# Kernel tuning notes

Measured on AMD Instinct MI355X. Metric: run time of the kernel, lower is better.

## Reference

```python
import jax, jax.numpy as jnp
import numpy as np

B, N, E, C, M = 4, 16384, 65536, 256, 64

def setup_inputs() -> dict:
    key = jax.random.key(0)
    ks = jax.random.split(key, 12)
    s = 1.0 / np.sqrt(C)
    return {
        'x': jax.random.normal(ks[0], (B, N, C), jnp.float32),
        'edge_attr': jax.random.normal(ks[1], (B, E, 1), jnp.float32),
        'edge_idx': jax.random.randint(ks[2], (B, E, 2), 0, N, jnp.int32),
        'W_fx': jax.random.normal(ks[3], (C, C), jnp.float32) * s,
        'b_fx': jnp.zeros((C,), jnp.float32),
        'W_x': jax.random.normal(ks[4], (C, C), jnp.float32) * s,
        'b_x': jnp.zeros((C,), jnp.float32),
        'W_slice': jax.random.normal(ks[5], (C, M), jnp.float32) * s,
        'b_slice': jnp.zeros((M,), jnp.float32),
        'temp_x': jnp.full((1, 1, M), 0.5, jnp.float32),
        'ph_x': jax.random.uniform(ks[6], (1, 1, C), jnp.float32) / C,
        'W_fedge': jax.random.normal(ks[7], (1, C), jnp.float32),
        'b_fedge': jnp.zeros((C,), jnp.float32),
        'temp_edge': jnp.full((1, 1, M), 0.5, jnp.float32),
        'W_eslice': jax.random.normal(ks[8], (M, M), jnp.float32) * (1.0 / np.sqrt(M)),
        'b_eslice': jnp.zeros((M,), jnp.float32),
        'ph_edge': jax.random.uniform(ks[9], (1, 1, C), jnp.float32) / C,
    }


def reference(x, edge_attr, edge_idx, W_fx, b_fx, W_x, b_x, W_slice, b_slice,
              temp_x, ph_x, W_fedge, b_fedge, temp_edge, W_eslice, b_eslice, ph_edge):
    # node path
    fx_mid = x @ W_fx + b_fx                                  # [B,N,C]
    x_mid = x @ W_x + b_x + ph_x                              # [B,N,C]
    logits = (x_mid @ W_slice + b_slice) / jnp.clip(temp_x, 0.01, 5.0)
    slice_weight = jax.nn.softmax(logits, axis=-1)            # [B,N,M]
    slice_norm = slice_weight.sum(axis=-2)[..., None]         # [B,M,1]
    slice_token = jnp.einsum('bnm,bnc->bmc', slice_weight, fx_mid)
    # edge path
    fedge_mid = edge_attr @ W_fedge + b_fedge + ph_edge       # [B,E,C]
    gather = jax.vmap(lambda sw, idx: sw[idx])                # per-batch node gather
    sw_sum = gather(slice_weight, edge_idx[:, :, 0]) + gather(slice_weight, edge_idx[:, :, 1])
    e_logits = (sw_sum / jnp.clip(temp_edge, 0.01, 5.0)) @ W_eslice + b_eslice
    edge_slice_weight = jax.nn.softmax(e_logits, axis=-1)     # [B,E,M]
    edge_slice_norm = edge_slice_weight.sum(axis=-2)[..., None]
    edge_slice_token = jnp.einsum('bnm,bnc->bmc', edge_slice_weight, fedge_mid)
    scale = x.shape[1] / edge_attr.shape[1]
    slice_token = slice_token + edge_slice_token * scale
    slice_norm = slice_norm + edge_slice_norm * scale
    slice_token = slice_token / (slice_norm + 1e-5)
    return (slice_token, slice_weight)
```

## Files before the change

kernel.cpp:

```cpp
#include <hip/hip_runtime.h>

#define BB 4
#define NN 16384
#define EE 65536
#define CC 256
#define MM 64

#define WS_NORM   0
#define WS_T1     256
#define WS_ESN    512
#define WS_BCOMB  768
#define WS_ITX    832
#define WS_ITE    896
#define WS_WES2   1024
#define WS_WCOMB  5120
#define WS_WES2T  13312
#define WS_SW2    21504
#define WS_SSUM   WS_SW2
#define WS_SPART  4215808

typedef __attribute__((ext_vector_type(8))) __bf16 bf16x8_t;
typedef __attribute__((ext_vector_type(4))) float f32x4_t;

static __device__ __forceinline__ unsigned short f2bf(float f) {
    unsigned int u = __float_as_uint(f);
    unsigned int r = (u + 0x7FFFu + ((u >> 16) & 1u)) >> 16;
    return (unsigned short)r;
}

__global__ __launch_bounds__(256) void kPP(const float* __restrict__ Wx,
                                           const float* __restrict__ Wsl,
                                           const float* __restrict__ bx,
                                           const float* __restrict__ phx,
                                           const float* __restrict__ bsl,
                                           const float* __restrict__ tx,
                                           const float* __restrict__ te,
                                           const float* __restrict__ Wes,
                                           float* __restrict__ ws) {
    __shared__ float row[256];
    __shared__ float part[4][64];
    const int tid = threadIdx.x;
    const int m = tid & 63, kq = tid >> 6;
    if (blockIdx.x < 256) {
        const int c = blockIdx.x;
        row[tid] = Wx[c * CC + tid];
        __syncthreads();
        float acc = 0.f;
#pragma unroll 8
        for (int kk = 0; kk < 64; ++kk) {
            int k = kq * 64 + kk;
            acc += row[k] * Wsl[k * MM + m];
        }
        part[kq][m] = acc;
        __syncthreads();
        if (tid < 64) {
            float v = part[0][tid] + part[1][tid] + part[2][tid] + part[3][tid];
            ((unsigned short*)(ws + WS_WCOMB))[tid * 256 + c] = f2bf(v);
        }
    } else {
#pragma unroll
        for (int i = 0; i < 3; ++i) ws[i * 256 + tid] = 0.f;
        row[tid] = bx[tid] + phx[tid];
        __syncthreads();
        float acc = 0.f;
#pragma unroll 8
        for (int kk = 0; kk < 64; ++kk) {
            int k = kq * 64 + kk;
            acc += row[k] * Wsl[k * MM + m];
        }
        part[kq][m] = acc;
        __syncthreads();
        if (tid < 64) {
            ws[WS_BCOMB + tid] = bsl[tid] +
                part[0][tid] + part[1][tid] + part[2][tid] + part[3][tid];
            ws[WS_ITX + tid] = 1.f / fminf(fmaxf(tx[tid], 0.01f), 5.f);
            ws[WS_ITE + tid] = 1.f / fminf(fmaxf(te[tid], 0.01f), 5.f);
        }
        unsigned short* w2t = (unsigned short*)(ws + WS_WES2T);
#pragma unroll
        for (int i = 0; i < 16; ++i) {
            int e = i * 256 + tid;
            int m2 = e >> 6, k2 = e & 63;
            float itk = 1.f / fminf(fmaxf(te[k2], 0.01f), 5.f);
            w2t[m2 * 64 + k2] = f2bf(itk * Wes[k2 * 64 + m2]);
        }
    }
}

__global__ __launch_bounds__(256, 2) void kN1(const float* __restrict__ x,
                                              const float* __restrict__ ws,
                                              float* __restrict__ out1,
                                              unsigned short* __restrict__ sw2b,
                                              float* __restrict__ norm_acc) {
    __shared__ float smem[17920];
    __shared__ float redn[4][64];
    __shared__ float bcs[64], itxs[64];
    unsigned short* smem_u = (unsigned short*)smem;
    float* swl = smem + 4096;
    const int tid = threadIdx.x;
    const int wv = tid >> 6, l = tid & 63;
    const int ln = l & 15, kg = l >> 4;
    const int row0 = blockIdx.x * 128;
    const int b = blockIdx.x >> 7;
    const int r = tid >> 2;
    const int h = tid & 3;

    if (tid < 64) { bcs[tid] = ws[WS_BCOMB + tid]; itxs[tid] = ws[WS_ITX + tid]; }

    const unsigned short* wct = (const unsigned short*)(ws + WS_WCOMB);
#pragma unroll
    for (int i = 0; i < 8; ++i) {
        int f8 = (i * 256 + tid) * 8;
        int m = f8 >> 8, k = f8 & 255;
        *(uint4*)&smem_u[m * 264 + k] = *(const uint4*)&wct[f8];
    }
    __syncthreads();

    f32x4_t acc[2][4];
#pragma unroll
    for (int i = 0; i < 2; ++i)
#pragma unroll
        for (int j = 0; j < 4; ++j) acc[i][j] = (f32x4_t){0.f, 0.f, 0.f, 0.f};

    for (int c0 = 0; c0 < CC; c0 += 32) {
        bf16x8_t bf[4];
#pragma unroll
        for (int mt = 0; mt < 4; ++mt)
            bf[mt] = *(const bf16x8_t*)&smem_u[(mt * 16 + ln) * 264 + c0 + kg * 8];
#pragma unroll
        for (int rt = 0; rt < 2; ++rt) {
            int arow = row0 + (wv * 2 + rt) * 16 + ln;
            const float* ap = x + (size_t)arow * CC + c0 + kg * 8;
            float4 p0 = *(const float4*)ap;
            float4 p1 = *(const float4*)(ap + 4);
            union { unsigned short u[8]; bf16x8_t v; } af;
            af.u[0] = f2bf(p0.x); af.u[1] = f2bf(p0.y);
            af.u[2] = f2bf(p0.z); af.u[3] = f2bf(p0.w);
            af.u[4] = f2bf(p1.x); af.u[5] = f2bf(p1.y);
            af.u[6] = f2bf(p1.z); af.u[7] = f2bf(p1.w);
#pragma unroll
            for (int mt = 0; mt < 4; ++mt)
                acc[rt][mt] = __builtin_amdgcn_mfma_f32_16x16x32_bf16(
                    af.v, bf[mt], acc[rt][mt], 0, 0, 0);
        }
    }
    __syncthreads();

#pragma unroll
    for (int rt = 0; rt < 2; ++rt)
#pragma unroll
        for (int mt = 0; mt < 4; ++mt)
#pragma unroll
            for (int j = 0; j < 4; ++j)
                swl[((wv * 2 + rt) * 16 + kg * 4 + j) * 68 + mt * 16 + ln] =
                    acc[rt][mt][j];
    {
        const unsigned short* w2tg = (const unsigned short*)(ws + WS_WES2T);
        int m2 = tid >> 2, k2 = (tid & 3) * 16;
        *(uint4*)&smem_u[m2 * 80 + k2] = *(const uint4*)&w2tg[m2 * 64 + k2];
        *(uint4*)&smem_u[m2 * 80 + k2 + 8] = *(const uint4*)&w2tg[m2 * 64 + k2 + 8];
    }
    __syncthreads();

    float sacc[2][16];
#pragma unroll
    for (int i = 0; i < 2; ++i)
#pragma unroll
        for (int q = 0; q < 4; ++q) {
            float4 v = *(float4*)&swl[(r + 64 * i) * 68 + h * 16 + q * 4];
            sacc[i][q * 4 + 0] = v.x; sacc[i][q * 4 + 1] = v.y;
            sacc[i][q * 4 + 2] = v.z; sacc[i][q * 4 + 3] = v.w;
        }
    float colsum[16];
#pragma unroll
    for (int j = 0; j < 16; ++j) colsum[j] = 0.f;
#pragma unroll
    for (int i = 0; i < 2; ++i) {
        float mx = -1e30f;
#pragma unroll
        for (int j = 0; j < 16; ++j) {
            int m = h * 16 + j;
            sacc[i][j] = (sacc[i][j] + bcs[m]) * itxs[m];
            mx = fmaxf(mx, sacc[i][j]);
        }
        mx = fmaxf(mx, __shfl_xor(mx, 1));
        mx = fmaxf(mx, __shfl_xor(mx, 2));
        float s = 0.f;
#pragma unroll
        for (int j = 0; j < 16; ++j) { sacc[i][j] = __expf(sacc[i][j] - mx); s += sacc[i][j]; }
        s += __shfl_xor(s, 1);
        s += __shfl_xor(s, 2);
        float inv = 1.f / s;
        int rl = r + 64 * i;
        int row = row0 + rl;
#pragma unroll
        for (int q = 0; q < 4; ++q) {
            float4 v = {sacc[i][q * 4 + 0] * inv, sacc[i][q * 4 + 1] * inv,
                        sacc[i][q * 4 + 2] * inv, sacc[i][q * 4 + 3] * inv};
            *(float4*)(out1 + (size_t)row * MM + h * 16 + q * 4) = v;
            *(float4*)&swl[rl * 68 + h * 16 + q * 4] = v;
#pragma unroll
            for (int j = 0; j < 4; ++j) colsum[q * 4 + j] += ((float*)&v)[j];
        }
    }
#pragma unroll
    for (int j = 0; j < 16; ++j) {
        colsum[j] += __shfl_xor(colsum[j], 4);
        colsum[j] += __shfl_xor(colsum[j], 8);
        colsum[j] += __shfl_xor(colsum[j], 16);
        colsum[j] += __shfl_xor(colsum[j], 32);
    }
    if (l < 4) {
#pragma unroll
        for (int j = 0; j < 16; ++j) redn[wv][h * 16 + j] = colsum[j];
    }
    __syncthreads();

    f32x4_t eacc[2][4];
#pragma unroll
    for (int i = 0; i < 2; ++i)
#pragma unroll
        for (int j = 0; j < 4; ++j) eacc[i][j] = (f32x4_t){0.f, 0.f, 0.f, 0.f};
#pragma unroll
    for (int ks = 0; ks < 2; ++ks) {
        bf16x8_t bfw[4];
#pragma unroll
        for (int mt = 0; mt < 4; ++mt)
            bfw[mt] = *(const bf16x8_t*)&smem_u[(mt * 16 + ln) * 80 + ks * 32 + kg * 8];
#pragma unroll
        for (int rt = 0; rt < 2; ++rt) {
            const float* ap = &swl[((wv * 2 + rt) * 16 + ln) * 68 + ks * 32 + kg * 8];
            float4 p0 = *(const float4*)ap;
            float4 p1 = *(const float4*)(ap + 4);
            union { unsigned short u[8]; bf16x8_t v; } af;
            af.u[0] = f2bf(p0.x); af.u[1] = f2bf(p0.y);
            af.u[2] = f2bf(p0.z); af.u[3] = f2bf(p0.w);
            af.u[4] = f2bf(p1.x); af.u[5] = f2bf(p1.y);
            af.u[6] = f2bf(p1.z); af.u[7] = f2bf(p1.w);
#pragma unroll
            for (int mt = 0; mt < 4; ++mt)
                eacc[rt][mt] = __builtin_amdgcn_mfma_f32_16x16x32_bf16(
                    af.v, bfw[mt], eacc[rt][mt], 0, 0, 0);
        }
    }
    {
        unsigned short* esb = (unsigned short*)(smem + 12800);
#pragma unroll
        for (int rt = 0; rt < 2; ++rt)
#pragma unroll
            for (int mt = 0; mt < 4; ++mt)
#pragma unroll
                for (int j = 0; j < 4; ++j)
                    esb[((wv * 2 + rt) * 16 + kg * 4 + j) * 80 + mt * 16 + ln] =
                        f2bf(eacc[rt][mt][j]);
    }
    __syncthreads();
    {
        const unsigned short* esb = (const unsigned short*)(smem + 12800);
        int row = tid >> 1, half = tid & 1;
        const uint4* src = (const uint4*)&esb[row * 80 + half * 32];
        uint4* dst = (uint4*)(sw2b + (size_t)(row0 + row) * MM + half * 32);
        dst[0] = src[0]; dst[1] = src[1]; dst[2] = src[2]; dst[3] = src[3];
    }

    if (tid < 64)
        atomicAdd(&norm_acc[b * MM + tid],
                  redn[0][tid] + redn[1][tid] + redn[2][tid] + redn[3][tid]);
}

__global__ __launch_bounds__(256, 4) void kEN2(const float* __restrict__ x,
                                               const float* __restrict__ sw,
                                               float* __restrict__ Spart,
                                               int PB, int rowsPB, int nb2,
                                               const float* __restrict__ eattr,
                                               const int* __restrict__ eidx,
                                               const unsigned short* __restrict__ sw2b,
                                               const float* __restrict__ bes,
                                               float* __restrict__ t1_acc,
                                               float* __restrict__ esn_acc) {
    __shared__ float smem[9280];
    const int tid = threadIdx.x;
    if ((int)blockIdx.x < nb2) {
        float* xs  = smem;
        float* sws = smem + 4608;
        const int bid = blockIdx.x;
        const int ch = bid & 1;
        const int p = (bid >> 1) % PB, b = (bid >> 1) / PB;
        const int base = b * NN + p * rowsPB;
        const int tm = tid >> 4, tc = tid & 15;
        const int m0 = tm * 4;
        const int c0 = tc * 8;

        float acc[4][8];
#pragma unroll
        for (int mi = 0; mi < 4; ++mi)
#pragma unroll
            for (int j = 0; j < 8; ++j) acc[mi][j] = 0.f;

        for (int r0 = 0; r0 < rowsPB; r0 += 32) {
            __syncthreads();
#pragma unroll
            for (int i = 0; i < 4; ++i) {
                int flat = i * 256 + tid;
                int r = flat >> 5, c = (flat & 31) * 4;
                float4 v = *(const float4*)(x + (size_t)(base + r0 + r) * CC + ch * 128 + c);
                *(float4*)&xs[r * 144 + c + ((c >> 5) << 2)] = v;
            }
#pragma unroll
            for (int i = 0; i < 2; ++i) {
                int flat = i * 256 + tid;
                int r = flat >> 4, c = (flat & 15) * 4;
                *(float4*)&sws[r * 64 + c] = *(const float4*)(sw + (size_t)(base + r0 + r) * MM + c);
            }
            __syncthreads();
#pragma unroll 2
            for (int r = 0; r < 32; ++r) {
                float4 s4 = *(float4*)&sws[r * 64 + m0];
#pragma unroll
                for (int q = 0; q < 2; ++q) {
                    int c = c0 + q * 4;
                    float4 xv = *(float4*)&xs[r * 144 + c + ((c >> 5) << 2)];
                    acc[0][q * 4 + 0] += s4.x * xv.x; acc[0][q * 4 + 1] += s4.x * xv.y;
                    acc[0][q * 4 + 2] += s4.x * xv.z; acc[0][q * 4 + 3] += s4.x * xv.w;
                    acc[1][q * 4 + 0] += s4.y * xv.x; acc[1][q * 4 + 1] += s4.y * xv.y;
                    acc[1][q * 4 + 2] += s4.y * xv.z; acc[1][q * 4 + 3] += s4.y * xv.w;
                    acc[2][q * 4 + 0] += s4.z * xv.x; acc[2][q * 4 + 1] += s4.z * xv.y;
                    acc[2][q * 4 + 2] += s4.z * xv.z; acc[2][q * 4 + 3] += s4.z * xv.w;
                    acc[3][q * 4 + 0] += s4.w * xv.x; acc[3][q * 4 + 1] += s4.w * xv.y;
                    acc[3][q * 4 + 2] += s4.w * xv.z; acc[3][q * 4 + 3] += s4.w * xv.w;
                }
            }
        }
        float* dst = Spart + (size_t)(b * PB + p) * MM * CC + ch * 128;
#pragma unroll
        for (int mi = 0; mi < 4; ++mi)
#pragma unroll
            for (int q = 0; q < 2; ++q) {
                float4 v = {acc[mi][q * 4 + 0], acc[mi][q * 4 + 1],
                            acc[mi][q * 4 + 2], acc[mi][q * 4 + 3]};
                *(float4*)(dst + (size_t)(m0 + mi) * CC + c0 + q * 4) = v;
            }
    } else {
        float* u    = smem;
        float* eav  = smem + 8448;
        float* redt = smem + 8704;
        float* redn = smem + 8960;
        float* bes_s = smem + 9216;
        const int w = tid >> 6, l = tid & 63;
        const int eg = ((int)blockIdx.x - nb2) * 256 + tid;
        const int b = eg >> 16;
        if (tid < 64) bes_s[tid] = bes[tid];
        const int2 idx = ((const int2*)eidx)[eg];
        const float ea = eattr[eg];
        const uint4* g0 = (const uint4*)(sw2b + (size_t)(b * NN + idx.x) * MM);
        const uint4* g1 = (const uint4*)(sw2b + (size_t)(b * NN + idx.y) * MM);
        eav[w * 64 + l] = ea;
        __syncthreads();

        float v[64];
#pragma unroll
        for (int q = 0; q < 8; ++q) {
            uint4 a = g0[q], c = g1[q];
            unsigned int au[4] = {a.x, a.y, a.z, a.w};
            unsigned int cu[4] = {c.x, c.y, c.z, c.w};
#pragma unroll
            for (int j = 0; j < 4; ++j) {
                int m = q * 8 + j * 2;
                v[m + 0] = __uint_as_float(au[j] << 16) + __uint_as_float(cu[j] << 16) + bes_s[m + 0];
                v[m + 1] = __uint_as_float(au[j] & 0xFFFF0000u) + __uint_as_float(cu[j] & 0xFFFF0000u) + bes_s[m + 1];
            }
        }
        float mx = -1e30f;
#pragma unroll
        for (int m = 0; m < 64; ++m) mx = fmaxf(mx, v[m]);
        float s = 0.f;
#pragma unroll
        for (int m = 0; m < 64; ++m) { v[m] = __expf(v[m] - mx); s += v[m]; }
        float inv = 1.f / s;

        const int ml = l & 31, rh = l >> 5;
#pragma unroll
        for (int ph = 0; ph < 2; ++ph) {
            __syncthreads();
#pragma unroll
            for (int j = 0; j < 32; ++j) u[w * 2112 + l * 33 + j] = v[ph * 32 + j] * inv;
            __syncthreads();
            float t = 0.f, n = 0.f;
#pragma unroll 8
            for (int rr = 0; rr < 32; ++rr) {
                int r = rh * 32 + rr;
                float e = u[w * 2112 + r * 33 + ml];
                n += e;
                t += e * eav[w * 64 + r];
            }
            t += __shfl_xor(t, 32);
            n += __shfl_xor(n, 32);
            if (l < 32) { redt[w * 64 + ph * 32 + l] = t; redn[w * 64 + ph * 32 + l] = n; }
        }
        __syncthreads();
        if (tid < 64) {
            atomicAdd(&t1_acc[b * 64 + tid],
                      redt[tid] + redt[64 + tid] + redt[128 + tid] + redt[192 + tid]);
            atomicAdd(&esn_acc[b * 64 + tid],
                      redn[tid] + redn[64 + tid] + redn[128 + tid] + redn[192 + tid]);
        }
    }
}

__global__ __launch_bounds__(256) void kR(const float* __restrict__ Spart,
                                          float* __restrict__ Ssum, int PB) {
    const int idx = blockIdx.x * 256 + threadIdx.x;
    const int b = idx >> 14;
    const int mc = idx & 16383;
    const float* sp = Spart + (size_t)b * PB * MM * CC + mc;
    float a0 = 0.f, a1 = 0.f, a2 = 0.f, a3 = 0.f;
    for (int p = 0; p < PB; p += 4) {
        a0 += sp[(size_t)(p + 0) * MM * CC];
        a1 += sp[(size_t)(p + 1) * MM * CC];
        a2 += sp[(size_t)(p + 2) * MM * CC];
        a3 += sp[(size_t)(p + 3) * MM * CC];
    }
    Ssum[idx] = (a0 + a1) + (a2 + a3);
}

__global__ __launch_bounds__(256) void kF2(const float* __restrict__ ws,
                                           const float* __restrict__ Wfx,
                                           const float* __restrict__ bfx,
                                           const float* __restrict__ Wfe,
                                           const float* __restrict__ bfe,
                                           const float* __restrict__ phe,
                                           float* __restrict__ out0) {
    __shared__ float srow[256];
    const int bid = blockIdx.x;
    const int b = bid >> 6, m = bid & 63;
    const int t = threadIdx.x;
    srow[t] = ws[WS_SSUM + (size_t)(b * MM + m) * CC + t];
    __syncthreads();
    float acc = 0.f;
#pragma unroll 8
    for (int k = 0; k < 256; ++k) acc += srow[k] * Wfx[k * CC + t];
    float nv  = ws[WS_NORM + b * 64 + m];
    float t1v = ws[WS_T1   + b * 64 + m];
    float ev  = ws[WS_ESN  + b * 64 + m];
    const float scale = (float)NN / (float)EE;
    float num = acc + nv * bfx[t] + scale * (t1v * Wfe[t] + ev * (bfe[t] + phe[t]));
    float den = nv + scale * ev + 1e-5f;
    out0[(size_t)(b * MM + m) * CC + t] = num / den;
}

extern "C" void kernel_launch(void* const* d_in, const int* in_sizes, int n_in,
                              void* d_out, int out_size, void* d_ws, size_t ws_size,
                              hipStream_t stream) {
    const float* x     = (const float*)d_in[0];
    const float* eattr = (const float*)d_in[1];
    const int*   eidx  = (const int*)d_in[2];
    const float* Wfx   = (const float*)d_in[3];
    const float* bfx   = (const float*)d_in[4];
    const float* Wx    = (const float*)d_in[5];
    const float* bx    = (const float*)d_in[6];
    const float* Wsl   = (const float*)d_in[7];
    const float* bsl   = (const float*)d_in[8];
    const float* tx    = (const float*)d_in[9];
    const float* phx   = (const float*)d_in[10];
    const float* Wfe   = (const float*)d_in[11];
    const float* bfe   = (const float*)d_in[12];
    const float* te    = (const float*)d_in[13];
    const float* Wes   = (const float*)d_in[14];
    const float* bes   = (const float*)d_in[15];
    const float* phe   = (const float*)d_in[16];

    float* out0 = (float*)d_out;
    float* out1 = out0 + (size_t)BB * MM * CC;
    float* ws   = (float*)d_ws;
    unsigned short* sw2b = (unsigned short*)(ws + WS_SW2);

    int PB = 64;
    while (PB > 8) {
        size_t need = (size_t)(WS_SPART + (size_t)BB * PB * MM * CC) * sizeof(float);
        if (need <= ws_size) break;
        PB >>= 1;
    }
    int rowsPB = NN / PB;
    int nb2 = BB * PB * 2;

    kPP<<<257, 256, 0, stream>>>(Wx, Wsl, bx, phx, bsl, tx, te, Wes, ws);
    kN1<<<512, 256, 0, stream>>>(x, ws, out1, sw2b, ws + WS_NORM);
    kEN2<<<nb2 + EE * BB / 256, 256, 0, stream>>>(x, out1, ws + WS_SPART, PB, rowsPB, nb2,
                                                  eattr, eidx, sw2b, bes,
                                                  ws + WS_T1, ws + WS_ESN);
    kR <<<1024, 256, 0, stream>>>(ws + WS_SPART, ws + WS_SSUM, PB);
    kF2<<<256, 256, 0, stream>>>(ws, Wfx, bfx, Wfe, bfe, phe, out0);
}
```

Before: 104.1 us.

## Use bf16 MFMA for slice-token accumulation in kEN2 node branch

Replaces the scalar FP32 FMA outer-product loop that accumulates slice_weight^T * x over node rows with MFMA 16x16x32 bf16 instructions. x and slice weights are converted to bf16 and stored transposed in shared memory with an XOR swizzle to avoid bank conflicts. Each wave computes a 64x32 output tile. This cuts ALU work in the node GEMM branch but gives up accuracy to bf16 inputs, and the scalar transposed LDS stores may be slower to stage.

```diff
diff --git a/kernel.cpp b/kernel.cpp
--- a/kernel.cpp
+++ b/kernel.cpp
@@ -281,65 +281,78 @@
     __shared__ float smem[9280];
     const int tid = threadIdx.x;
     if ((int)blockIdx.x < nb2) {
-        float* xs  = smem;
-        float* sws = smem + 4608;
+        unsigned short* xT = (unsigned short*)smem;
+        unsigned short* sT = (unsigned short*)(smem + 2560);
         const int bid = blockIdx.x;
         const int ch = bid & 1;
         const int p = (bid >> 1) % PB, b = (bid >> 1) / PB;
         const int base = b * NN + p * rowsPB;
-        const int tm = tid >> 4, tc = tid & 15;
-        const int m0 = tm * 4;
-        const int c0 = tc * 8;
-
-        float acc[4][8];
-#pragma unroll
-        for (int mi = 0; mi < 4; ++mi)
-#pragma unroll
-            for (int j = 0; j < 8; ++j) acc[mi][j] = 0.f;
+        const int wv = tid >> 6, l = tid & 63;
+        const int ln = l & 15, kg = l >> 4;
+        const int ct0 = wv * 2;
+
+        f32x4_t acc[2][4];
+#pragma unroll
+        for (int i = 0; i < 2; ++i)
+#pragma unroll
+            for (int j = 0; j < 4; ++j) acc[i][j] = (f32x4_t){0.f, 0.f, 0.f, 0.f};
 
         for (int r0 = 0; r0 < rowsPB; r0 += 32) {
             __syncthreads();
 #pragma unroll
             for (int i = 0; i < 4; ++i) {
                 int flat = i * 256 + tid;
-                int r = flat >> 5, c = (flat & 31) * 4;
-                float4 v = *(const float4*)(x + (size_t)(base + r0 + r) * CC + ch * 128 + c);
-                *(float4*)&xs[r * 144 + c + ((c >> 5) << 2)] = v;
+                int rr = flat >> 5, c = (flat & 31) * 4;
+                float4 v = *(const float4*)(x + (size_t)(base + r0 + rr) * CC + ch * 128 + c);
+                int key = (c >> 2) & 3;
+                int off = ((rr >> 3) ^ key) * 8 + (rr & 7);
+                xT[(c + 0) * 40 + off] = f2bf(v.x);
+                xT[(c + 1) * 40 + off] = f2bf(v.y);
+                xT[(c + 2) * 40 + off] = f2bf(v.z);
+                xT[(c + 3) * 40 + off] = f2bf(v.w);
             }
 #pragma unroll
             for (int i = 0; i < 2; ++i) {
                 int flat = i * 256 + tid;
-                int r = flat >> 4, c = (flat & 15) * 4;
-                *(float4*)&sws[r * 64 + c] = *(const float4*)(sw + (size_t)(base + r0 + r) * MM + c);
+                int rr = flat >> 4, m = (flat & 15) * 4;
+                float4 v = *(const float4*)(sw + (size_t)(base + r0 + rr) * MM + m);
+                int key = (m >> 2) & 3;
+                int off = ((rr >> 3) ^ key) * 8 + (rr & 7);
+                sT[(m + 0) * 40 + off] = f2bf(v.x);
+                sT[(m + 1) * 40 + off] = f2bf(v.y);
+                sT[(m + 2) * 40 + off] = f2bf(v.z);
+                sT[(m + 3) * 40 + off] = f2bf(v.w);
             }
             __syncthreads();
-#pragma unroll 2
-            for (int r = 0; r < 32; ++r) {
-                float4 s4 = *(float4*)&sws[r * 64 + m0];
-#pragma unroll
-                for (int q = 0; q < 2; ++q) {
-                    int c = c0 + q * 4;
-                    float4 xv = *(float4*)&xs[r * 144 + c + ((c >> 5) << 2)];
-                    acc[0][q * 4 + 0] += s4.x * xv.x; acc[0][q * 4 + 1] += s4.x * xv.y;
-                    acc[0][q * 4 + 2] += s4.x * xv.z; acc[0][q * 4 + 3] += s4.x * xv.w;
-                    acc[1][q * 4 + 0] += s4.y * xv.x; acc[1][q * 4 + 1] += s4.y * xv.y;
-                    acc[1][q * 4 + 2] += s4.y * xv.z; acc[1][q * 4 + 3] += s4.y * xv.w;
-                    acc[2][q * 4 + 0] += s4.z * xv.x; acc[2][q * 4 + 1] += s4.z * xv.y;
-                    acc[2][q * 4 + 2] += s4.z * xv.z; acc[2][q * 4 + 3] += s4.z * xv.w;
-                    acc[3][q * 4 + 0] += s4.w * xv.x; acc[3][q * 4 + 1] += s4.w * xv.y;
-                    acc[3][q * 4 + 2] += s4.w * xv.z; acc[3][q * 4 + 3] += s4.w * xv.w;
+            bf16x8_t afr[4];
+#pragma unroll
+            for (int mt = 0; mt < 4; ++mt) {
+                int m = mt * 16 + ln;
+                int chunk = kg ^ ((m >> 2) & 3);
+                afr[mt] = *(const bf16x8_t*)&sT[m * 40 + chunk * 8];
+            }
+#pragma unroll
+            for (int ct = 0; ct < 2; ++ct) {
+                int c = (ct0 + ct) * 16 + ln;
+                int chunk = kg ^ ((c >> 2) & 3);
+                bf16x8_t bfr = *(const bf16x8_t*)&xT[c * 40 + chunk * 8];
+#pragma unroll
+                for (int mt = 0; mt < 4; ++mt)
+                    acc[ct][mt] = __builtin_amdgcn_mfma_f32_16x16x32_bf16(
+                        afr[mt], bfr, acc[ct][mt], 0, 0, 0);
+            }
+        }
+        float* dst = Spart + (size_t)(b * PB + p) * MM * CC + ch * 128;
+#pragma unroll
+        for (int ct = 0; ct < 2; ++ct)
+#pragma unroll
+            for (int mt = 0; mt < 4; ++mt)
+#pragma unroll
+                for (int j = 0; j < 4; ++j) {
+                    int m = mt * 16 + kg * 4 + j;
+                    int c = (ct0 + ct) * 16 + ln;
+                    dst[(size_t)m * CC + c] = acc[ct][mt][j];
                 }
-            }
-        }
-        float* dst = Spart + (size_t)(b * PB + p) * MM * CC + ch * 128;
-#pragma unroll
-        for (int mi = 0; mi < 4; ++mi)
-#pragma unroll
-            for (int q = 0; q < 2; ++q) {
-                float4 v = {acc[mi][q * 4 + 0], acc[mi][q * 4 + 1],
-                            acc[mi][q * 4 + 2], acc[mi][q * 4 + 3]};
-                *(float4*)(dst + (size_t)(m0 + mi) * CC + c0 + q * 4) = v;
-            }
     } else {
         float* u    = smem;
         float* eav  = smem + 8448;
```

Measured after the change: 98.01 us. 5.8% less time.
